# Kernel tuning notes

Measured on AMD Instinct MI355X. Metric: run time of the kernel, lower is better.

Reference implementation:

```python
import jax, jax.numpy as jnp
import numpy as np

B, T, F, D, H, L = 4, 1024, 128, 512, 8, 4
DFF = 4 * D
NE, MD = 16, 20
HD = D // H
SCALE = 1.0 / HD ** 0.5


def _ln(x, w, b):
    m = jnp.mean(x, axis=-1, keepdims=True)
    v = jnp.mean((x - m) ** 2, axis=-1, keepdims=True)
    return (x - m) * jax.lax.rsqrt(v + 1e-5) * w + b


def setup_inputs() -> dict:
    key = jax.random.key(0)
    ks = jax.random.split(key, 16)
    rn = lambda k, shape: jax.random.normal(k, shape, jnp.float32) * 0.02
    return {
        'node_features': jax.random.normal(ks[0], (B, T, F), jnp.float32),
        'centrality': jax.random.uniform(ks[1], (B, T), jnp.float32),
        'edge_types': jax.random.randint(ks[2], (B, T, T), 0, NE),
        'sp_dist': jax.random.randint(ks[3], (B, T, T), 0, MD + 1),
        'node_W': rn(ks[4], (F, D)), 'node_b': jnp.zeros((D,), jnp.float32),
        'cent_W': rn(ks[5], (D,)), 'cent_b': jnp.zeros((D,), jnp.float32),
        'edge_emb': rn(ks[6], (NE, H)), 'dist_emb': rn(ks[7], (MD + 1, H)),
        'ln1_w': jnp.ones((L, D), jnp.float32), 'ln1_b': jnp.zeros((L, D), jnp.float32),
        'q_W': rn(ks[8], (L, D, D)), 'q_b': jnp.zeros((L, D), jnp.float32),
        'k_W': rn(ks[9], (L, D, D)), 'k_b': jnp.zeros((L, D), jnp.float32),
        'v_W': rn(ks[10], (L, D, D)), 'v_b': jnp.zeros((L, D), jnp.float32),
        'o_W': rn(ks[11], (L, D, D)), 'o_b': jnp.zeros((L, D), jnp.float32),
        'ln2_w': jnp.ones((L, D), jnp.float32), 'ln2_b': jnp.zeros((L, D), jnp.float32),
        'f1_W': rn(ks[12], (L, D, DFF)), 'f1_b': jnp.zeros((L, DFF), jnp.float32),
        'f2_W': rn(ks[13], (L, DFF, D)), 'f2_b': jnp.zeros((L, D), jnp.float32),
    }


def _forward(node_features, centrality, edge_types, sp_dist,
             node_W, node_b, cent_W, cent_b, edge_emb, dist_emb,
             ln1_w, ln1_b, q_W, q_b, k_W, k_b, v_W, v_b, o_W, o_b,
             ln2_w, ln2_b, f1_W, f1_b, f2_W, f2_b):
    # node embedding + centrality encoding
    h = node_features @ node_W + node_b                      # [B,T,D]
    h = h + centrality[..., None] * cent_W + cent_b          # Linear(1,D)
    # Graphormer attention bias: [B,T,T,H] -> [B,H,T,T]
    sp = jnp.clip(sp_dist, 0, MD)
    attn_bias = (edge_emb[edge_types] + dist_emb[sp]).transpose(0, 3, 1, 2)

    def step(h, p):
        l1w, l1b, qW, qb, kW, kb, vW, vb, oW, ob, l2w, l2b, w1, b1, w2, b2 = p
        x = _ln(h, l1w, l1b)
        q = (x @ qW + qb).reshape(B, T, H, HD)
        k = (x @ kW + kb).reshape(B, T, H, HD)
        v = (x @ vW + vb).reshape(B, T, H, HD)
        scores = jnp.einsum('bihd,bjhd->bhij', q, k) * SCALE + attn_bias
        attn = jax.nn.softmax(scores, axis=-1)
        o = jnp.einsum('bhij,bjhd->bihd', attn, v).reshape(B, T, D)
        h = h + (o @ oW + ob)                                # dropout in eval mode
        x2 = _ln(h, l2w, l2b)
        h = h + (jax.nn.silu(x2 @ w1 + b1) @ w2 + b2)
        return h, None

    layer_params = (ln1_w, ln1_b, q_W, q_b, k_W, k_b, v_W, v_b, o_W, o_b,
                    ln2_w, ln2_b, f1_W, f1_b, f2_W, f2_b)
    h, _ = jax.lax.scan(step, h, layer_params)
    return h


def reference(node_features, centrality, edge_types, sp_dist,
              node_W, node_b, cent_W, cent_b, edge_emb, dist_emb,
              ln1_w, ln1_b, q_W, q_b, k_W, k_b, v_W, v_b, o_W, o_b,
              ln2_w, ln2_b, f1_W, f1_b, f2_W, f2_b):
    return _forward(node_features, centrality, edge_types, sp_dist,
                    node_W, node_b, cent_W, cent_b, edge_emb, dist_emb,
                    ln1_w, ln1_b, q_W, q_b, k_W, k_b, v_W, v_b, o_W, o_b,
                    ln2_w, ln2_b, f1_W, f1_b, f2_W, f2_b)
```

## Files before the change

### kernel.cpp

```cpp
#include <hip/hip_runtime.h>
#include <cstddef>
#include <cstdint>

#define B_    4
#define T_    1024
#define F_    128
#define D_    512
#define H_    8
#define L_    4
#define DFF_  2048
#define HD_   64
#define SCALE_ 0.125f
#define LOG2E_ 1.4426950408889634f
#define CL2E_  (SCALE_ * LOG2E_)

typedef __attribute__((ext_vector_type(8))) short bf16x8;
typedef __attribute__((ext_vector_type(4))) float f32x4;

#define AS1(p) ((const __attribute__((address_space(1))) void*)(p))
#define AS3(p) ((__attribute__((address_space(3))) void*)(p))

__device__ __forceinline__ short f2bf(float f) {
    unsigned u = __float_as_uint(f);
    u += 0x7FFFu + ((u >> 16) & 1u);
    return (short)(u >> 16);
}

__global__ __launch_bounds__(256) void cast_nf_k(
    const float* __restrict__ src, short* __restrict__ dst)
{
    const int i = (blockIdx.x * 256 + threadIdx.x) << 2;
    const float4 v = *(const float4*)(src + i);
    short4 o = make_short4(f2bf(v.x), f2bf(v.y), f2bf(v.z), f2bf(v.w));
    *(short4*)(dst + i) = o;
}

__global__ __launch_bounds__(256) void ln_k(
    const float* __restrict__ X, const float* __restrict__ w,
    const float* __restrict__ b, short* __restrict__ Y)
{
    const int row = blockIdx.x;
    const int tid = threadIdx.x;
    const float* xr = X + (size_t)row * D_;
    const float v0 = xr[tid];
    const float v1 = xr[tid + 256];
    float s  = v0 + v1;
    float s2 = v0 * v0 + v1 * v1;
#pragma unroll
    for (int off = 1; off < 64; off <<= 1) {
        s  += __shfl_xor(s,  off);
        s2 += __shfl_xor(s2, off);
    }
    __shared__ float ss[4], ss2[4];
    if ((tid & 63) == 0) { ss[tid >> 6] = s; ss2[tid >> 6] = s2; }
    __syncthreads();
    s  = ss[0]  + ss[1]  + ss[2]  + ss[3];
    s2 = ss2[0] + ss2[1] + ss2[2] + ss2[3];
    const float mean = s * (1.f / D_);
    const float var  = s2 * (1.f / D_) - mean * mean;
    const float r    = rsqrtf(var + 1e-5f);
    short* yr = Y + (size_t)row * D_;
    yr[tid]       = f2bf((v0 - mean) * r * w[tid]       + b[tid]);
    yr[tid + 256] = f2bf((v1 - mean) * r * w[tid + 256] + b[tid + 256]);
}

__global__ __launch_bounds__(256) void transpose_all_k(
    const float* __restrict__ qW, const float* __restrict__ kW,
    const float* __restrict__ vW, const float* __restrict__ oW,
    const float* __restrict__ f1W, const float* __restrict__ f2W,
    const float* __restrict__ nW,
    short* __restrict__ WqkvT, short* __restrict__ WoT,
    short* __restrict__ Wf1T, short* __restrict__ Wf2T,
    short* __restrict__ nWt)
{
    const int id = blockIdx.y;
    const float* src; short* dst; int K, N;
    if (id < 12) {
        const int l = id / 3, which = id % 3;
        const float* s3 = (which == 0) ? qW : (which == 1) ? kW : vW;
        src = s3 + (size_t)l * D_ * D_;
        dst = WqkvT + ((size_t)l * 3 + which) * D_ * D_;
        K = D_; N = D_;
    } else if (id < 16) {
        const int l = id - 12;
        src = oW + (size_t)l * D_ * D_;  dst = WoT + (size_t)l * D_ * D_;
        K = D_; N = D_;
    } else if (id < 20) {
        const int l = id - 16;
        src = f1W + (size_t)l * D_ * DFF_;  dst = Wf1T + (size_t)l * DFF_ * D_;
        K = D_; N = DFF_;
    } else if (id < 24) {
        const int l = id - 20;
        src = f2W + (size_t)l * DFF_ * D_;  dst = Wf2T + (size_t)l * D_ * DFF_;
        K = DFF_; N = D_;
    } else {
        src = nW; dst = nWt; K = F_; N = D_;
    }
    const int ntiles = (K >> 5) * (N >> 5);
    if ((int)blockIdx.x >= ntiles) return;
    const int nt = N >> 5;
    const int k0 = (blockIdx.x / nt) << 5, n0 = (blockIdx.x % nt) << 5;

    __shared__ float t[32][33];
    const int c = threadIdx.x, r0 = threadIdx.y;
#pragma unroll
    for (int i = 0; i < 32; i += 8)
        t[r0 + i][c] = src[(size_t)(k0 + r0 + i) * N + n0 + c];
    __syncthreads();
#pragma unroll
    for (int i = 0; i < 32; i += 8)
        dst[(size_t)(n0 + r0 + i) * K + k0 + c] = f2bf(t[c][r0 + i]);
}

__global__ __launch_bounds__(256) void fuse_bias_k(
    const float* __restrict__ qb, const float* __restrict__ kb,
    const float* __restrict__ vb, float* __restrict__ dst)
{
    const int i = blockIdx.x * 256 + threadIdx.x;
    const int l = i / 1536, c = i % 1536;
    float v;
    if (c < 512)       v = qb[l * 512 + c];
    else if (c < 1024) v = kb[l * 512 + c - 512];
    else               v = vb[l * 512 + c - 1024];
    dst[i] = v;
}

__global__ __launch_bounds__(256) void bias_k(
    const int* __restrict__ et, const int* __restrict__ sp,
    const float* __restrict__ ee, const float* __restrict__ de,
    short* __restrict__ biasT)
{
    __shared__ float eeS[16][8], deS[21][8];
    const int tid = threadIdx.x;
    if (tid < 128) eeS[tid >> 3][tid & 7] = ee[tid];
    for (int t = tid; t < 168; t += 256)
        deS[t >> 3][t & 7] = de[t];
    __syncthreads();
    const int gid = blockIdx.x * 256 + tid;
    const int j4  = (gid & 255) << 2;
    const int bi  = gid >> 8;
    const size_t base = (size_t)bi * T_ + j4;
    const int4 e = *(const int4*)(et + base);
    const int4 s = *(const int4*)(sp + base);
    const int b = bi >> 10, i = bi & 1023;
    const int ex[4] = {e.x, e.y, e.z, e.w};
    const int sx[4] = {min(s.x, 20), min(s.y, 20), min(s.z, 20), min(s.w, 20)};
#pragma unroll
    for (int h = 0; h < 8; ++h) {
        short4 o;
        o.x = f2bf((eeS[ex[0]][h] + deS[sx[0]][h]) * LOG2E_);
        o.y = f2bf((eeS[ex[1]][h] + deS[sx[1]][h]) * LOG2E_);
        o.z = f2bf((eeS[ex[2]][h] + deS[sx[2]][h]) * LOG2E_);
        o.w = f2bf((eeS[ex[3]][h] + deS[sx[3]][h]) * LOG2E_);
        *(short4*)(biasT + ((size_t)((b * H_ + h) * T_ + i)) * T_ + j4) = o;
    }
}

__global__ __launch_bounds__(256) void embed_mm_k(
    const short* __restrict__ A, const short* __restrict__ Wt,
    const float* __restrict__ nb, const float* __restrict__ cb,
    const float* __restrict__ cW, const float* __restrict__ cent,
    float* __restrict__ C)
{
    const int K = F_, N = D_;
    __shared__ short As[128 * 32];
    __shared__ short Bs[64 * 32];
    const int tid  = threadIdx.x;
    const int lane = tid & 63, wv = tid >> 6;
    const int bm = blockIdx.y << 7, bn = blockIdx.x << 6;
    const int wm = (wv & 1) << 6, wn = (wv >> 1) << 5;

    const int c0 = (wv << 6) + lane;
    const int m0 = c0 >> 2, q0 = (c0 & 3) ^ ((m0 >> 1) & 3);
    const int c1 = 256 + c0;
    const int m1 = c1 >> 2, q1 = (c1 & 3) ^ ((m1 >> 1) & 3);

    const short* gA0 = A  + (size_t)(bm + m0) * K + (q0 << 3);
    const short* gA1 = A  + (size_t)(bm + m1) * K + (q1 << 3);
    const short* gB0 = Wt + (size_t)(bn + m0) * K + (q0 << 3);

    f32x4 acc[4][2];
#pragma unroll
    for (int i = 0; i < 4; ++i)
#pragma unroll
        for (int j = 0; j < 2; ++j)
            acc[i][j] = (f32x4){0.f, 0.f, 0.f, 0.f};

    const int fm = lane & 15, fq = lane >> 4;
    int caddr[4], baddr[2];
#pragma unroll
    for (int t = 0; t < 4; ++t) {
        const int rowA = wm + (t << 4) + fm;
        caddr[t] = ((rowA << 2) + (fq ^ ((rowA >> 1) & 3))) << 3;
    }
#pragma unroll
    for (int t = 0; t < 2; ++t) {
        const int rowB = wn + (t << 4) + fm;
        baddr[t] = ((rowB << 2) + (fq ^ ((rowB >> 1) & 3))) << 3;
    }

    for (int k0 = 0; k0 < K; k0 += 32) {
        __builtin_amdgcn_global_load_lds(AS1(gA0), AS3(As + (wv << 9)),        16, 0, 0);
        __builtin_amdgcn_global_load_lds(AS1(gA1), AS3(As + 2048 + (wv << 9)), 16, 0, 0);
        __builtin_amdgcn_global_load_lds(AS1(gB0), AS3(Bs + (wv << 9)),        16, 0, 0);
        gA0 += 32; gA1 += 32; gB0 += 32;
        __syncthreads();

        bf16x8 af[4], bf[2];
#pragma unroll
        for (int t = 0; t < 4; ++t) af[t] = *(const bf16x8*)(As + caddr[t]);
#pragma unroll
        for (int t = 0; t < 2; ++t) bf[t] = *(const bf16x8*)(Bs + baddr[t]);
#pragma unroll
        for (int i = 0; i < 4; ++i)
#pragma unroll
            for (int j = 0; j < 2; ++j)
                acc[i][j] = __builtin_amdgcn_mfma_f32_16x16x32_bf16(
                    af[i], bf[j], acc[i][j], 0, 0, 0);
        __syncthreads();
    }

    const int col0 = bn + wn + fm;
    const int row0 = bm + wm + (fq << 2);
#pragma unroll
    for (int j = 0; j < 2; ++j) {
        const int colg = col0 + (j << 4);
        const float bb = nb[colg] + cb[colg];
        const float cw = cW[colg];
#pragma unroll
        for (int i = 0; i < 4; ++i) {
#pragma unroll
            for (int r = 0; r < 4; ++r) {
                const int rowg = row0 + (i << 4) + r;
                C[(size_t)rowg * N + colg] = acc[i][j][r] + bb + cent[rowg] * cw;
            }
        }
    }
}

template <int OUTM, int ACT, int RES>
__global__ __launch_bounds__(256) void mm_k(
    const short* __restrict__ A, const short* __restrict__ Wt,
    const float* __restrict__ bias, const float* __restrict__ R,
    void* __restrict__ Cv, short* __restrict__ VtOut, int M, int N, int K)
{
    __shared__ short As[128 * 32];
    __shared__ short Bs[128 * 32];
    const int tid  = threadIdx.x;
    const int lane = tid & 63, wv = tid >> 6;
    const int bm = blockIdx.y << 7, bn = blockIdx.x << 7;
    const int wm = (wv & 1) << 6, wn = (wv >> 1) << 6;

    const int c0 = (wv << 6) + lane;
    const int m0 = c0 >> 2, q0 = (c0 & 3) ^ ((m0 >> 1) & 3);
    const int c1 = 256 + c0;
    const int m1 = c1 >> 2, q1 = (c1 & 3) ^ ((m1 >> 1) & 3);

    const short* gA0 = A  + (size_t)(bm + m0) * K + (q0 << 3);
    const short* gA1 = A  + (size_t)(bm + m1) * K + (q1 << 3);
    const short* gB0 = Wt + (size_t)(bn + m0) * K + (q0 << 3);
    const short* gB1 = Wt + (size_t)(bn + m1) * K + (q1 << 3);

    f32x4 acc[4][4];
#pragma unroll
    for (int i = 0; i < 4; ++i)
#pragma unroll
        for (int j = 0; j < 4; ++j)
            acc[i][j] = (f32x4){0.f, 0.f, 0.f, 0.f};

    const int fm = lane & 15, fq = lane >> 4;
    int caddr[4], baddr[4];
#pragma unroll
    for (int t = 0; t < 4; ++t) {
        const int rowA = wm + (t << 4) + fm;
        caddr[t] = ((rowA << 2) + (fq ^ ((rowA >> 1) & 3))) << 3;
        const int rowB = wn + (t << 4) + fm;
        baddr[t] = ((rowB << 2) + (fq ^ ((rowB >> 1) & 3))) << 3;
    }

    for (int k0 = 0; k0 < K; k0 += 32) {
        __builtin_amdgcn_global_load_lds(AS1(gA0), AS3(As + (wv << 9)),        16, 0, 0);
        __builtin_amdgcn_global_load_lds(AS1(gA1), AS3(As + 2048 + (wv << 9)), 16, 0, 0);
        __builtin_amdgcn_global_load_lds(AS1(gB0), AS3(Bs + (wv << 9)),        16, 0, 0);
        __builtin_amdgcn_global_load_lds(AS1(gB1), AS3(Bs + 2048 + (wv << 9)), 16, 0, 0);
        gA0 += 32; gA1 += 32; gB0 += 32; gB1 += 32;
        __syncthreads();

        bf16x8 af[4], bf[4];
#pragma unroll
        for (int t = 0; t < 4; ++t) {
            af[t] = *(const bf16x8*)(As + caddr[t]);
            bf[t] = *(const bf16x8*)(Bs + baddr[t]);
        }
#pragma unroll
        for (int i = 0; i < 4; ++i)
#pragma unroll
            for (int j = 0; j < 4; ++j)
                acc[i][j] = __builtin_amdgcn_mfma_f32_16x16x32_bf16(
                    af[i], bf[j], acc[i][j], 0, 0, 0);
        __syncthreads();
    }

    const int col0 = bn + wn + fm;
    const int row0 = bm + wm + (fq << 2);
    float* Cf = (float*)Cv;
    short* Cb = (short*)Cv;
#pragma unroll
    for (int j = 0; j < 4; ++j) {
        const int colg = col0 + (j << 4);
        const float bb = bias[colg];
#pragma unroll
        for (int i = 0; i < 4; ++i) {
#pragma unroll
            for (int r = 0; r < 4; ++r) {
                const int rowg = row0 + (i << 4) + r;
                float v = acc[i][j][r] + bb;
                if (ACT) v = v / (1.f + __expf(-v));
                if (OUTM == 2) {
                    if (colg < 1024) {
                        Cb[(size_t)rowg * 1024 + colg] = f2bf(v);
                    } else {
                        const int da = colg - 1024;
                        const int hh = da >> 6, dd = da & 63;
                        const int bb2 = rowg >> 10, tt = rowg & 1023;
                        VtOut[((size_t)(bb2 * H_ + hh) * 64 + dd) * T_ + tt] = f2bf(v);
                    }
                } else {
                    const size_t off = (size_t)rowg * N + colg;
                    if (RES) v += R[off];
                    if (OUTM == 1) Cb[off] = f2bf(v);
                    else           Cf[off] = v;
                }
            }
        }
    }
}

__global__ __launch_bounds__(256) void mm64_k(
    const short* __restrict__ A, const short* __restrict__ Wt,
    const float* __restrict__ bias, const float* __restrict__ R,
    float* __restrict__ C, int M, int N, int K)
{
    __shared__ short As[128 * 32];
    __shared__ short Bs[64 * 32];
    const int tid  = threadIdx.x;
    const int lane = tid & 63, wv = tid >> 6;
    const int bm = blockIdx.y << 7, bn = blockIdx.x << 6;
    const int wm = (wv & 1) << 6, wn = (wv >> 1) << 5;

    const int c0 = (wv << 6) + lane;
    const int m0 = c0 >> 2, q0 = (c0 & 3) ^ ((m0 >> 1) & 3);
    const int c1 = 256 + c0;
    const int m1 = c1 >> 2, q1 = (c1 & 3) ^ ((m1 >> 1) & 3);

    const short* gA0 = A  + (size_t)(bm + m0) * K + (q0 << 3);
    const short* gA1 = A  + (size_t)(bm + m1) * K + (q1 << 3);
    const short* gB0 = Wt + (size_t)(bn + m0) * K + (q0 << 3);

    f32x4 acc[4][2];
#pragma unroll
    for (int i = 0; i < 4; ++i)
#pragma unroll
        for (int j = 0; j < 2; ++j)
            acc[i][j] = (f32x4){0.f, 0.f, 0.f, 0.f};

    const int fm = lane & 15, fq = lane >> 4;
    int caddr[4], baddr[2];
#pragma unroll
    for (int t = 0; t < 4; ++t) {
        const int rowA = wm + (t << 4) + fm;
        caddr[t] = ((rowA << 2) + (fq ^ ((rowA >> 1) & 3))) << 3;
    }
#pragma unroll
    for (int t = 0; t < 2; ++t) {
        const int rowB = wn + (t << 4) + fm;
        baddr[t] = ((rowB << 2) + (fq ^ ((rowB >> 1) & 3))) << 3;
    }

    for (int k0 = 0; k0 < K; k0 += 32) {
        __builtin_amdgcn_global_load_lds(AS1(gA0), AS3(As + (wv << 9)),        16, 0, 0);
        __builtin_amdgcn_global_load_lds(AS1(gA1), AS3(As + 2048 + (wv << 9)), 16, 0, 0);
        __builtin_amdgcn_global_load_lds(AS1(gB0), AS3(Bs + (wv << 9)),        16, 0, 0);
        gA0 += 32; gA1 += 32; gB0 += 32;
        __syncthreads();

        bf16x8 af[4], bf[2];
#pragma unroll
        for (int t = 0; t < 4; ++t) af[t] = *(const bf16x8*)(As + caddr[t]);
#pragma unroll
        for (int t = 0; t < 2; ++t) bf[t] = *(const bf16x8*)(Bs + baddr[t]);
#pragma unroll
        for (int i = 0; i < 4; ++i)
#pragma unroll
            for (int j = 0; j < 2; ++j)
                acc[i][j] = __builtin_amdgcn_mfma_f32_16x16x32_bf16(
                    af[i], bf[j], acc[i][j], 0, 0, 0);
        __syncthreads();
    }

    const int col0 = bn + wn + fm;
    const int row0 = bm + wm + (fq << 2);
#pragma unroll
    for (int j = 0; j < 2; ++j) {
        const int colg = col0 + (j << 4);
        const float bb = bias[colg];
#pragma unroll
        for (int i = 0; i < 4; ++i) {
#pragma unroll
            for (int r = 0; r < 4; ++r) {
                const int rowg = row0 + (i << 4) + r;
                const size_t off = (size_t)rowg * N + colg;
                C[off] = acc[i][j][r] + bb + R[off];
            }
        }
    }
}

__global__ __launch_bounds__(256) void flash_k(
    const short* __restrict__ QKb, const short* __restrict__ Vt,
    const short* __restrict__ biasT, float* __restrict__ Opart,
    float* __restrict__ Lpart)
{
    const int tid = threadIdx.x;
    const int bx = blockIdx.x;
    const int it = bx >> 1, split = bx & 1;
    const int i0 = it << 6;
    const int h  = blockIdx.y;
    const int b  = blockIdx.z;
    const int lane = tid & 63, w = tid >> 6;
    const int fm = lane & 15, q = lane >> 4;

    __shared__ short Ks[4096];
    __shared__ short Vs[4096];
    __shared__ short Ps[64][72];

    const short* qp = QKb + (size_t)(b * T_ + i0 + (w << 4) + fm) * 1024 + (h << 6) + (q << 3);
    const bf16x8 aq0 = *(const bf16x8*)(qp);
    const bf16x8 aq1 = *(const bf16x8*)(qp + 32);

    const int s0 = (w << 6) + lane, r0 = s0 >> 3, cc0 = (s0 & 7) ^ (r0 & 7);
    const int s1 = 256 + s0,        r1 = s1 >> 3, cc1 = (s1 & 7) ^ (r1 & 7);
    const short* gK0 = QKb + (size_t)(b * T_ + r0) * 1024 + 512 + (h << 6) + (cc0 << 3);
    const short* gK1 = QKb + (size_t)(b * T_ + r1) * 1024 + 512 + (h << 6) + (cc1 << 3);
    const short* gV0 = Vt + ((size_t)((b * H_ + h) << 6) + r0) * T_ + (cc0 << 3);
    const short* gV1 = Vt + ((size_t)((b * H_ + h) << 6) + r1) * T_ + (cc1 << 3);

    int fAddr[4][2];
#pragma unroll
    for (int t = 0; t < 4; ++t) {
        const int row = (t << 4) + fm;
#pragma unroll
        for (int ks = 0; ks < 2; ++ks)
            fAddr[t][ks] = (row << 6) + (((q + (ks << 2)) ^ (row & 7)) << 3);
    }

    const short* bptr = biasT +
        ((size_t)(b * H_ + h) * T_ + i0 + (w << 4) + (q << 2)) * T_ + fm;

    const short oneb = 0x3F80;
    const bf16x8 ones = {oneb, oneb, oneb, oneb, oneb, oneb, oneb, oneb};

    f32x4 accO[4];
#pragma unroll
    for (int dt = 0; dt < 4; ++dt) accO[dt] = (f32x4){0.f, 0.f, 0.f, 0.f};
    f32x4 accL = (f32x4){0.f, 0.f, 0.f, 0.f};

    const int irow = b * T_ + i0 + (w << 4) + (q << 2);
    short* psW = &Ps[(w << 4) + (q << 2)][fm];
    const short* psR = &Ps[(w << 4) + fm][q << 3];

    const int jbeg = split << 9, jend = jbeg + 512;
    for (int j0 = jbeg; j0 < jend; j0 += 64) {
        __syncthreads();
        __builtin_amdgcn_global_load_lds(AS1(gK0 + (size_t)j0 * 1024), AS3(Ks + (s0 << 3)), 16, 0, 0);
        __builtin_amdgcn_global_load_lds(AS1(gK1 + (size_t)j0 * 1024), AS3(Ks + (s1 << 3)), 16, 0, 0);
        __builtin_amdgcn_global_load_lds(AS1(gV0 + j0), AS3(Vs + (s0 << 3)), 16, 0, 0);
        __builtin_amdgcn_global_load_lds(AS1(gV1 + j0), AS3(Vs + (s1 << 3)), 16, 0, 0);

        float bb[4][4];
#pragma unroll
        for (int r = 0; r < 4; ++r)
#pragma unroll
            for (int jt = 0; jt < 4; ++jt) {
                const unsigned u = *(const unsigned short*)(bptr + (size_t)r * T_ + j0 + (jt << 4));
                bb[r][jt] = __uint_as_float(u << 16);
            }
        __syncthreads();

        f32x4 s[4];
#pragma unroll
        for (int jt = 0; jt < 4; ++jt) s[jt] = (f32x4){0.f, 0.f, 0.f, 0.f};
#pragma unroll
        for (int jt = 0; jt < 4; ++jt) {
            const bf16x8 k0 = *(const bf16x8*)(Ks + fAddr[jt][0]);
            const bf16x8 k1 = *(const bf16x8*)(Ks + fAddr[jt][1]);
            s[jt] = __builtin_amdgcn_mfma_f32_16x16x32_bf16(aq0, k0, s[jt], 0, 0, 0);
            s[jt] = __builtin_amdgcn_mfma_f32_16x16x32_bf16(aq1, k1, s[jt], 0, 0, 0);
        }

#pragma unroll
        for (int r = 0; r < 4; ++r)
#pragma unroll
            for (int jt = 0; jt < 4; ++jt) {
                const float p = __builtin_amdgcn_exp2f(fmaf(s[jt][r], CL2E_, bb[r][jt]));
                psW[(size_t)r * 72 + (jt << 4)] = f2bf(p);
            }

#pragma unroll
        for (int ks = 0; ks < 2; ++ks) {
            const bf16x8 ap = *(const bf16x8*)(psR + (ks << 5));
            accL = __builtin_amdgcn_mfma_f32_16x16x32_bf16(ap, ones, accL, 0, 0, 0);
#pragma unroll
            for (int dt = 0; dt < 4; ++dt) {
                const bf16x8 bv = *(const bf16x8*)(Vs + fAddr[dt][ks]);
                accO[dt] = __builtin_amdgcn_mfma_f32_16x16x32_bf16(ap, bv, accO[dt], 0, 0, 0);
            }
        }
    }

    float* obase = Opart + (size_t)split * B_ * T_ * D_;
#pragma unroll
    for (int r = 0; r < 4; ++r) {
        float* op = obase + (size_t)(irow + r) * D_ + (h << 6) + fm;
#pragma unroll
        for (int dt = 0; dt < 4; ++dt)
            op[dt << 4] = accO[dt][r];
    }
    if (fm == 0) {
#pragma unroll
        for (int r = 0; r < 4; ++r)
            Lpart[(size_t)split * B_ * T_ * H_ + (size_t)(irow + r) * H_ + h] = accL[r];
    }
}

__global__ __launch_bounds__(256) void combine_k(
    const float* __restrict__ Opart, const float* __restrict__ Lpart,
    short* __restrict__ Ob)
{
    const int gid = blockIdx.x * 256 + threadIdx.x;
    const int d4  = (gid & 127) << 2;
    const int row = gid >> 7;
    const int h   = d4 >> 6;
    const float l = Lpart[(size_t)row * H_ + h] +
                    Lpart[(size_t)B_ * T_ * H_ + (size_t)row * H_ + h];
    const float inv = 1.f / l;
    const size_t o = (size_t)row * D_ + d4;
    const float4 a = *(const float4*)(Opart + o);
    const float4 c = *(const float4*)(Opart + (size_t)B_ * T_ * D_ + o);
    short4 r = make_short4(f2bf((a.x + c.x) * inv), f2bf((a.y + c.y) * inv),
                           f2bf((a.z + c.z) * inv), f2bf((a.w + c.w) * inv));
    *(short4*)(Ob + o) = r;
}

extern "C" void kernel_launch(void* const* d_in, const int* in_sizes, int n_in,
                              void* d_out, int out_size, void* d_ws, size_t ws_size,
                              hipStream_t stream)
{
    (void)in_sizes; (void)n_in; (void)out_size; (void)ws_size;

    const float* nf   = (const float*)d_in[0];
    const float* cent = (const float*)d_in[1];
    const int*   et   = (const int*)  d_in[2];
    const int*   sp   = (const int*)  d_in[3];
    const float* nW   = (const float*)d_in[4];
    const float* nb   = (const float*)d_in[5];
    const float* cW   = (const float*)d_in[6];
    const float* cb   = (const float*)d_in[7];
    const float* ee   = (const float*)d_in[8];
    const float* de   = (const float*)d_in[9];
    const float* ln1w = (const float*)d_in[10];
    const float* ln1b = (const float*)d_in[11];
    const float* qW   = (const float*)d_in[12];
    const float* qb   = (const float*)d_in[13];
    const float* kW   = (const float*)d_in[14];
    const float* kb   = (const float*)d_in[15];
    const float* vW   = (const float*)d_in[16];
    const float* vb   = (const float*)d_in[17];
    const float* oW   = (const float*)d_in[18];
    const float* ob   = (const float*)d_in[19];
    const float* ln2w = (const float*)d_in[20];
    const float* ln2b = (const float*)d_in[21];
    const float* f1W  = (const float*)d_in[22];
    const float* f1b  = (const float*)d_in[23];
    const float* f2W  = (const float*)d_in[24];
    const float* f2b  = (const float*)d_in[25];

    const int M = B_ * T_;
    char* p = (char*)d_ws;
    float* Hbuf  = (float*)p;  p += (size_t)M * D_ * 4;
    short* QKb   = (short*)p;  p += (size_t)M * 1024 * 2;
    short* Vt    = (short*)p;  p += (size_t)B_ * H_ * 64 * T_ * 2;
    float* biasf = (float*)p;  p += (size_t)L_ * 3 * D_ * 4;
    short* Xbuf  = (short*)p;  p += (size_t)M * D_ * 2;
    short* Ob    = (short*)p;  p += (size_t)M * D_ * 2;
    short* FF    = (short*)p;  p += (size_t)M * DFF_ * 2;
    short* biasT = (short*)p;  p += (size_t)B_ * H_ * T_ * T_ * 2;
    short* WqkvT = (short*)p;  p += (size_t)L_ * 3 * D_ * D_ * 2;
    short* WoT   = (short*)p;  p += (size_t)L_ * D_ * D_ * 2;
    short* Wf1T  = (short*)p;  p += (size_t)L_ * DFF_ * D_ * 2;
    short* Wf2T  = (short*)p;  p += (size_t)L_ * D_ * DFF_ * 2;
    short* nfb   = (short*)p;  p += (size_t)M * F_ * 2;
    short* nWt   = (short*)p;  p += (size_t)D_ * F_ * 2;
    float* Opart = (float*)p;  p += (size_t)2 * M * D_ * 4;
    float* Lpart = (float*)p;  p += (size_t)2 * M * H_ * 4;

    float* out = (float*)d_out;

    transpose_all_k<<<dim3(1024, 25), dim3(32, 8), 0, stream>>>(
        qW, kW, vW, oW, f1W, f2W, nW, WqkvT, WoT, Wf1T, Wf2T, nWt);
    cast_nf_k<<<dim3(M * F_ / 1024), dim3(256), 0, stream>>>(nf, nfb);
    fuse_bias_k<<<dim3(L_ * 3 * D_ / 256), dim3(256), 0, stream>>>(qb, kb, vb, biasf);
    bias_k<<<dim3(B_ * T_ * T_ / 1024), dim3(256), 0, stream>>>(et, sp, ee, de, biasT);
    embed_mm_k<<<dim3(D_ / 64, M / 128), dim3(256), 0, stream>>>(
        nfb, nWt, nb, cb, cW, cent, Hbuf);

    const dim3 blk(256);
    const dim3 gQKV(3 * D_ / 128, M / 128);
    const dim3 gO64(D_ / 64,      M / 128);
    const dim3 gF1 (DFF_ / 128,   M / 128);
    const dim3 gAttn(2 * T_ / 64, H_, B_);
    const dim3 gCmb(M * D_ / 1024);

    for (int l = 0; l < L_; ++l) {
        const size_t bOff  = (size_t)l * D_;
        const size_t b1Off = (size_t)l * DFF_;

        ln_k<<<dim3(M), blk, 0, stream>>>(Hbuf, ln1w + bOff, ln1b + bOff, Xbuf);

        mm_k<2, 0, 0><<<gQKV, blk, 0, stream>>>(
            Xbuf, WqkvT + (size_t)l * 3 * D_ * D_, biasf + (size_t)l * 3 * D_,
            nullptr, QKb, Vt, M, 3 * D_, D_);

        flash_k<<<gAttn, blk, 0, stream>>>(QKb, Vt, biasT, Opart, Lpart);
        combine_k<<<gCmb, blk, 0, stream>>>(Opart, Lpart, Ob);

        mm64_k<<<gO64, blk, 0, stream>>>(
            Ob, WoT + (size_t)l * D_ * D_, ob + bOff, Hbuf, Hbuf, M, D_, D_);

        ln_k<<<dim3(M), blk, 0, stream>>>(Hbuf, ln2w + bOff, ln2b + bOff, Xbuf);

        mm_k<1, 1, 0><<<gF1, blk, 0, stream>>>(
            Xbuf, Wf1T + (size_t)l * DFF_ * D_, f1b + b1Off, nullptr, FF, nullptr, M, DFF_, D_);

        float* cdst = (l == L_ - 1) ? out : Hbuf;
        mm64_k<<<gO64, blk, 0, stream>>>(
            FF, Wf2T + (size_t)l * D_ * DFF_, f2b + bOff, Hbuf, cdst, M, D_, DFF_);
    }
}
```

Before: 701.0 us.

## Merge prep kernels, use 64-wide QKV GEMM, stage attention bias via LDS

```diff
diff --git a/kernel.cpp b/kernel.cpp
--- a/kernel.cpp
+++ b/kernel.cpp
@@ -24,15 +24,6 @@
     unsigned u = __float_as_uint(f);
     u += 0x7FFFu + ((u >> 16) & 1u);
     return (short)(u >> 16);
-}
-
-__global__ __launch_bounds__(256) void cast_nf_k(
-    const float* __restrict__ src, short* __restrict__ dst)
-{
-    const int i = (blockIdx.x * 256 + threadIdx.x) << 2;
-    const float4 v = *(const float4*)(src + i);
-    short4 o = make_short4(f2bf(v.x), f2bf(v.y), f2bf(v.z), f2bf(v.w));
-    *(short4*)(dst + i) = o;
 }
 
 __global__ __launch_bounds__(256) void ln_k(
@@ -112,31 +103,39 @@
         dst[(size_t)(n0 + r0 + i) * K + k0 + c] = f2bf(t[c][r0 + i]);
 }
 
-__global__ __launch_bounds__(256) void fuse_bias_k(
-    const float* __restrict__ qb, const float* __restrict__ kb,
-    const float* __restrict__ vb, float* __restrict__ dst)
-{
-    const int i = blockIdx.x * 256 + threadIdx.x;
-    const int l = i / 1536, c = i % 1536;
-    float v;
-    if (c < 512)       v = qb[l * 512 + c];
-    else if (c < 1024) v = kb[l * 512 + c - 512];
-    else               v = vb[l * 512 + c - 1024];
-    dst[i] = v;
-}
-
-__global__ __launch_bounds__(256) void bias_k(
+__global__ __launch_bounds__(256) void prep_k(
     const int* __restrict__ et, const int* __restrict__ sp,
     const float* __restrict__ ee, const float* __restrict__ de,
-    short* __restrict__ biasT)
-{
+    short* __restrict__ biasT,
+    const float* __restrict__ nf, short* __restrict__ nfb,
+    const float* __restrict__ qb, const float* __restrict__ kb,
+    const float* __restrict__ vb, float* __restrict__ biasf)
+{
+    const int bid = blockIdx.x;
+    const int tid = threadIdx.x;
+    if (bid >= 4096) {
+        if (bid < 4608) {
+            const int i = (((bid - 4096) << 8) + tid) << 2;
+            const float4 v = *(const float4*)(nf + i);
+            *(short4*)(nfb + i) =
+                make_short4(f2bf(v.x), f2bf(v.y), f2bf(v.z), f2bf(v.w));
+        } else {
+            const int i = ((bid - 4608) << 8) + tid;
+            const int l = i / 1536, c = i % 1536;
+            float v;
+            if (c < 512)       v = qb[l * 512 + c];
+            else if (c < 1024) v = kb[l * 512 + c - 512];
+            else               v = vb[l * 512 + c - 1024];
+            biasf[i] = v;
+        }
+        return;
+    }
     __shared__ float eeS[16][8], deS[21][8];
-    const int tid = threadIdx.x;
     if (tid < 128) eeS[tid >> 3][tid & 7] = ee[tid];
     for (int t = tid; t < 168; t += 256)
         deS[t >> 3][t & 7] = de[t];
     __syncthreads();
-    const int gid = blockIdx.x * 256 + tid;
+    const int gid = bid * 256 + tid;
     const int j4  = (gid & 255) << 2;
     const int bi  = gid >> 8;
     const size_t base = (size_t)bi * T_ + j4;
@@ -242,7 +241,7 @@
 __global__ __launch_bounds__(256) void mm_k(
     const short* __restrict__ A, const short* __restrict__ Wt,
     const float* __restrict__ bias, const float* __restrict__ R,
-    void* __restrict__ Cv, short* __restrict__ VtOut, int M, int N, int K)
+    void* __restrict__ Cv, int M, int N, int K)
 {
     __shared__ short As[128 * 32];
     __shared__ short Bs[128 * 32];
@@ -316,31 +315,21 @@
                 const int rowg = row0 + (i << 4) + r;
                 float v = acc[i][j][r] + bb;
                 if (ACT) v = v / (1.f + __expf(-v));
-                if (OUTM == 2) {
-                    if (colg < 1024) {
-                        Cb[(size_t)rowg * 1024 + colg] = f2bf(v);
-                    } else {
-                        const int da = colg - 1024;
-                        const int hh = da >> 6, dd = da & 63;
-                        const int bb2 = rowg >> 10, tt = rowg & 1023;
-                        VtOut[((size_t)(bb2 * H_ + hh) * 64 + dd) * T_ + tt] = f2bf(v);
-                    }
-                } else {
-                    const size_t off = (size_t)rowg * N + colg;
-                    if (RES) v += R[off];
-                    if (OUTM == 1) Cb[off] = f2bf(v);
-                    else           Cf[off] = v;
-                }
+                const size_t off = (size_t)rowg * N + colg;
+                if (RES) v += R[off];
+                if (OUTM == 1) Cb[off] = f2bf(v);
+                else           Cf[off] = v;
             }
         }
     }
 }
 
-__global__ __launch_bounds__(256) void mm64_k(
+__global__ __launch_bounds__(256) void qkv64_k(
     const short* __restrict__ A, const short* __restrict__ Wt,
-    const float* __restrict__ bias, const float* __restrict__ R,
-    float* __restrict__ C, int M, int N, int K)
-{
+    const float* __restrict__ bias, short* __restrict__ QKb,
+    short* __restrict__ VtOut)
+{
+    const int K = D_;
     __shared__ short As[128 * 32];
     __shared__ short Bs[64 * 32];
     const int tid  = threadIdx.x;
@@ -409,8 +398,15 @@
 #pragma unroll
             for (int r = 0; r < 4; ++r) {
                 const int rowg = row0 + (i << 4) + r;
-                const size_t off = (size_t)rowg * N + colg;
-                C[off] = acc[i][j][r] + bb + R[off];
+                const float v = acc[i][j][r] + bb;
+                if (colg < 1024) {
+                    QKb[(size_t)rowg * 1024 + colg] = f2bf(v);
+                } else {
+                    const int da = colg - 1024;
+                    const int hh = da >> 6, dd = da & 63;
+                    const int bb2 = rowg >> 10, tt = rowg & 1023;
+                    VtOut[((size_t)(bb2 * H_ + hh) * 64 + dd) * T_ + tt] = f2bf(v);
+                }
             }
         }
     }
@@ -432,6 +428,7 @@
 
     __shared__ short Ks[4096];
     __shared__ short Vs[4096];
+    __shared__ short Bsh[4096];
     __shared__ short Ps[64][72];
 
     const short* qp = QKb + (size_t)(b * T_ + i0 + (w << 4) + fm) * 1024 + (h << 6) + (q << 3);
@@ -444,6 +441,8 @@
     const short* gK1 = QKb + (size_t)(b * T_ + r1) * 1024 + 512 + (h << 6) + (cc1 << 3);
     const short* gV0 = Vt + ((size_t)((b * H_ + h) << 6) + r0) * T_ + (cc0 << 3);
     const short* gV1 = Vt + ((size_t)((b * H_ + h) << 6) + r1) * T_ + (cc1 << 3);
+    const short* gB0 = biasT + ((size_t)(b * H_ + h) * T_ + i0 + r0) * T_ + (cc0 << 3);
+    const short* gB1 = biasT + ((size_t)(b * H_ + h) * T_ + i0 + r1) * T_ + (cc1 << 3);
 
     int fAddr[4][2];
 #pragma unroll
@@ -454,8 +453,15 @@
             fAddr[t][ks] = (row << 6) + (((q + (ks << 2)) ^ (row & 7)) << 3);
     }
 
-    const short* bptr = biasT +
-        ((size_t)(b * H_ + h) * T_ + i0 + (w << 4) + (q << 2)) * T_ + fm;
+    int bAddr[4][4];
+#pragma unroll
+    for (int r = 0; r < 4; ++r) {
+        const int rowL = (w << 4) + (q << 2) + r;
+#pragma unroll
+        for (int jt = 0; jt < 4; ++jt)
+            bAddr[r][jt] = (rowL << 6) +
+                (((((jt << 1) + (fm >> 3))) ^ (rowL & 7)) << 3) + (fm & 7);
+    }
 
     const short oneb = 0x3F80;
     const bf16x8 ones = {oneb, oneb, oneb, oneb, oneb, oneb, oneb, oneb};
@@ -476,15 +482,8 @@
         __builtin_amdgcn_global_load_lds(AS1(gK1 + (size_t)j0 * 1024), AS3(Ks + (s1 << 3)), 16, 0, 0);
         __builtin_amdgcn_global_load_lds(AS1(gV0 + j0), AS3(Vs + (s0 << 3)), 16, 0, 0);
         __builtin_amdgcn_global_load_lds(AS1(gV1 + j0), AS3(Vs + (s1 << 3)), 16, 0, 0);
-
-        float bb[4][4];
-#pragma unroll
-        for (int r = 0; r < 4; ++r)
-#pragma unroll
-            for (int jt = 0; jt < 4; ++jt) {
-                const unsigned u = *(const unsigned short*)(bptr + (size_t)r * T_ + j0 + (jt << 4));
-                bb[r][jt] = __uint_as_float(u << 16);
-            }
+        __builtin_amdgcn_global_load_lds(AS1(gB0 + j0), AS3(Bsh + (s0 << 3)), 16, 0, 0);
+        __builtin_amdgcn_global_load_lds(AS1(gB1 + j0), AS3(Bsh + (s1 << 3)), 16, 0, 0);
         __syncthreads();
 
         f32x4 s[4];
@@ -502,7 +501,9 @@
         for (int r = 0; r < 4; ++r)
 #pragma unroll
             for (int jt = 0; jt < 4; ++jt) {
-                const float p = __builtin_amdgcn_exp2f(fmaf(s[jt][r], CL2E_, bb[r][jt]));
+                const unsigned u = *(const unsigned short*)(Bsh + bAddr[r][jt]);
+                const float bb = __uint_as_float(u << 16);
+                const float p = __builtin_amdgcn_exp2f(fmaf(s[jt][r], CL2E_, bb));
                 psW[(size_t)r * 72 + (jt << 4)] = f2bf(p);
             }
 
@@ -550,6 +551,86 @@
     short4 r = make_short4(f2bf((a.x + c.x) * inv), f2bf((a.y + c.y) * inv),
                            f2bf((a.z + c.z) * inv), f2bf((a.w + c.w) * inv));
     *(short4*)(Ob + o) = r;
+}
+
+__global__ __launch_bounds__(256) void mm64_k(
+    const short* __restrict__ A, const short* __restrict__ Wt,
+    const float* __restrict__ bias, const float* __restrict__ R,
+    float* __restrict__ C, int M, int N, int K)
+{
+    __shared__ short As[128 * 32];
+    __shared__ short Bs[64 * 32];
+    const int tid  = threadIdx.x;
+    const int lane = tid & 63, wv = tid >> 6;
+    const int bm = blockIdx.y << 7, bn = blockIdx.x << 6;
+    const int wm = (wv & 1) << 6, wn = (wv >> 1) << 5;
+
+    const int c0 = (wv << 6) + lane;
+    const int m0 = c0 >> 2, q0 = (c0 & 3) ^ ((m0 >> 1) & 3);
+    const int c1 = 256 + c0;
+    const int m1 = c1 >> 2, q1 = (c1 & 3) ^ ((m1 >> 1) & 3);
+
+    const short* gA0 = A  + (size_t)(bm + m0) * K + (q0 << 3);
+    const short* gA1 = A  + (size_t)(bm + m1) * K + (q1 << 3);
+    const short* gB0 = Wt + (size_t)(bn + m0) * K + (q0 << 3);
+
+    f32x4 acc[4][2];
+#pragma unroll
+    for (int i = 0; i < 4; ++i)
+#pragma unroll
+        for (int j = 0; j < 2; ++j)
+            acc[i][j] = (f32x4){0.f, 0.f, 0.f, 0.f};
+
+    const int fm = lane & 15, fq = lane >> 4;
+    int caddr[4], baddr[2];
+#pragma unroll
+    for (int t = 0; t < 4; ++t) {
+        const int rowA = wm + (t << 4) + fm;
+        caddr[t] = ((rowA << 2) + (fq ^ ((rowA >> 1) & 3))) << 3;
+    }
+#pragma unroll
+    for (int t = 0; t < 2; ++t) {
+        const int rowB = wn + (t << 4) + fm;
+        baddr[t] = ((rowB << 2) + (fq ^ ((rowB >> 1) & 3))) << 3;
+    }
+
+    for (int k0 = 0; k0 < K; k0 += 32) {
+        __builtin_amdgcn_global_load_lds(AS1(gA0), AS3(As + (wv << 9)),        16, 0, 0);
+        __builtin_amdgcn_global_load_lds(AS1(gA1), AS3(As + 2048 + (wv << 9)), 16, 0, 0);
+        __builtin_amdgcn_global_load_lds(AS1(gB0), AS3(Bs + (wv << 9)),        16, 0, 0);
+        gA0 += 32; gA1 += 32; gB0 += 32;
+        __syncthreads();
+
+        bf16x8 af[4], bf[2];
+#pragma unroll
+        for (int t = 0; t < 4; ++t) af[t] = *(const bf16x8*)(As + caddr[t]);
+#pragma unroll
+        for (int t = 0; t < 2; ++t) bf[t] = *(const bf16x8*)(Bs + baddr[t]);
+#pragma unroll
+        for (int i = 0; i < 4; ++i)
+#pragma unroll
+            for (int j = 0; j < 2; ++j)
+                acc[i][j] = __builtin_amdgcn_mfma_f32_16x16x32_bf16(
+                    af[i], bf[j], acc[i][j], 0, 0, 0);
+        __syncthreads();
+    }
+
+    const int col0 = bn + wn + fm;
+    const int row0 = bm + wm + (fq << 2);
+#pragma unroll
+    for (int j = 0; j < 2; ++j) {
+        const int colg = col0 + (j << 4);
+        const float bb = bias[colg];
+#pragma unroll
+        for (int i = 0; i < 4; ++i) {
+#pragma unroll
+            for (int r = 0; r < 4; ++r) {
+                const int rowg = row0 + (i << 4) + r;
+                const size_t off = (size_t)rowg * N + colg;
+                C[off] = acc[i][j][r] + bb + R[off];
+            }
+        }
+    }
 }
 
 extern "C" void kernel_launch(void* const* d_in, const int* in_sizes, int n_in,
@@ -608,16 +689,15 @@
 
     transpose_all_k<<<dim3(1024, 25), dim3(32, 8), 0, stream>>>(
         qW, kW, vW, oW, f1W, f2W, nW, WqkvT, WoT, Wf1T, Wf2T, nWt);
-    cast_nf_k<<<dim3(M * F_ / 1024), dim3(256), 0, stream>>>(nf, nfb);
-    fuse_bias_k<<<dim3(L_ * 3 * D_ / 256), dim3(256), 0, stream>>>(qb, kb, vb, biasf);
-    bias_k<<<dim3(B_ * T_ * T_ / 1024), dim3(256), 0, stream>>>(et, sp, ee, de, biasT);
+    prep_k<<<dim3(4632), dim3(256), 0, stream>>>(
+        et, sp, ee, de, biasT, nf, nfb, qb, kb, vb, biasf);
     embed_mm_k<<<dim3(D_ / 64, M / 128), dim3(256), 0, stream>>>(
         nfb, nWt, nb, cb, cW, cent, Hbuf);
 
     const dim3 blk(256);
-    const dim3 gQKV(3 * D_ / 128, M / 128);
-    const dim3 gO64(D_ / 64,      M / 128);
-    const dim3 gF1 (DFF_ / 128,   M / 128);
+    const dim3 gQKV(3 * D_ / 64, M / 128);
+    const dim3 gO64(D_ / 64,     M / 128);
+    const dim3 gF1 (DFF_ / 128,  M / 128);
     const dim3 gAttn(2 * T_ / 64, H_, B_);
     const dim3 gCmb(M * D_ / 1024);
 
@@ -627,9 +707,9 @@
 
         ln_k<<<dim3(M), blk, 0, stream>>>(Hbuf, ln1w + bOff, ln1b + bOff, Xbuf);
 
-        mm_k<2, 0, 0><<<gQKV, blk, 0, stream>>>(
+        qkv64_k<<<gQKV, blk, 0, stream>>>(
             Xbuf, WqkvT + (size_t)l * 3 * D_ * D_, biasf + (size_t)l * 3 * D_,
-            nullptr, QKb, Vt, M, 3 * D_, D_);
+            QKb, Vt);
 
         flash_k<<<gAttn, blk, 0, stream>>>(QKb, Vt, biasT, Opart, Lpart);
         combine_k<<<gCmb, blk, 0, stream>>>(Opart, Lpart, Ob);
@@ -640,7 +720,7 @@
         ln_k<<<dim3(M), blk, 0, stream>>>(Hbuf, ln2w + bOff, ln2b + bOff, Xbuf);
 
         mm_k<1, 1, 0><<<gF1, blk, 0, stream>>>(
-            Xbuf, Wf1T + (size_t)l * DFF_ * D_, f1b + b1Off, nullptr, FF, nullptr, M, DFF_, D_);
+            Xbuf, Wf1T + (size_t)l * DFF_ * D_, f1b + b1Off, nullptr, FF, M, DFF_, D_);
 
         float* cdst = (l == L_ - 1) ? out : Hbuf;
         mm64_k<<<gO64, blk, 0, stream>>>(
```

Result: no change. 691.6 us (-1.3%).
